# Kernel tuning notes

Measured on AMD Instinct MI355X. Metric: run time of the kernel, lower is better.

Reference implementation:

```python
import jax, jax.numpy as jnp
import numpy as np

B, S, D = 2, 2048, 2048
H = 16
DH = D // H  # 128, head dim for q, also the single kv head dim
ROPE_BASE = 10000.0


def _rope_cos_sin(seq_len, dim, dtype):
    inv_freq = 1.0 / (ROPE_BASE ** (jnp.arange(0, dim, 2, dtype=jnp.float32) / dim))
    t = jnp.arange(seq_len, dtype=jnp.float32)
    freqs = jnp.outer(t, inv_freq)            # [S, dim/2]
    emb = jnp.concatenate([freqs, freqs], -1)  # [S, dim]
    return jnp.cos(emb).astype(dtype), jnp.sin(emb).astype(dtype)


def _rotate_half(x):
    x1, x2 = x[..., : x.shape[-1] // 2], x[..., x.shape[-1] // 2 :]
    return jnp.concatenate([-x2, x1], axis=-1)


def setup_inputs() -> dict:
    key = jax.random.key(0)
    ks = jax.random.split(key, 7)
    s = 0.02
    return {
        "x": jax.random.normal(ks[0], (B, S, D), jnp.float32),
        "q_weight": jax.random.normal(ks[1], (H * DH, D), jnp.float32) * s,
        "q_bias": jax.random.normal(ks[2], (H * DH,), jnp.float32) * s,
        "kv_weight": jax.random.normal(ks[3], (2 * DH, D), jnp.float32) * s,
        "kv_bias": jax.random.normal(ks[4], (2 * DH,), jnp.float32) * s,
        "o_weight": jax.random.normal(ks[5], (D, H * DH), jnp.float32) * s,
        "o_bias": jax.random.normal(ks[6], (D,), jnp.float32) * s,
    }


def reference(x, q_weight, q_bias, kv_weight, kv_bias, o_weight, o_bias):
    b, s, d = x.shape
    # fused-style MQA projections (torch F.linear: y = x @ W.T + b)
    q = x @ q_weight.T + q_bias                      # [B,S,H*DH]
    kv = x @ kv_weight.T + kv_bias                   # [B,S,2*DH]
    q = q.reshape(b, s, H, DH)
    k, v = kv[..., :DH], kv[..., DH:]                # [B,S,DH] single kv head

    # rotary embedding (GPT-NeoX / rotate_half style) on q and k
    cos, sin = _rope_cos_sin(s, DH, x.dtype)         # [S,DH]
    q = q * cos[None, :, None, :] + _rotate_half(q) * sin[None, :, None, :]
    k = k * cos[None, :, :] + _rotate_half(k) * sin[None, :, :]

    # causal MQA attention (flash_attn_varlen with full masks == dense causal)
    scale = 1.0 / jnp.sqrt(jnp.asarray(DH, x.dtype))
    scores = jnp.einsum("bqhd,bkd->bhqk", q, k) * scale   # [B,H,S,S]
    causal = jnp.tril(jnp.ones((s, s), bool))
    scores = jnp.where(causal[None, None], scores, jnp.asarray(-1e9, x.dtype))
    probs = jax.nn.softmax(scores, axis=-1)
    attn = jnp.einsum("bhqk,bkd->bqhd", probs, v)         # [B,S,H,DH]

    out = attn.reshape(b, s, H * DH) @ o_weight.T + o_bias
    return out
```

## Files before the change

### kernel.cpp

```cpp
#include <hip/hip_runtime.h>
#include <math.h>

constexpr int Bb  = 2;
constexpr int Ss  = 2048;
constexpr int Dd  = 2048;
constexpr int Hh  = 16;
constexpr int DHd = 128;
constexpr int BS  = Bb * Ss;
constexpr int NQKV = 2304;

typedef __bf16 bf16x8 __attribute__((ext_vector_type(8)));
typedef float  f32x4  __attribute__((ext_vector_type(4)));

static __device__ __forceinline__ unsigned short f2bf(float f) {
  union { float f; unsigned int u; } a; a.f = f;
  unsigned int u = a.u;
  unsigned int r = (u + 0x7fffu + ((u >> 16) & 1u)) >> 16;
  return (unsigned short)r;
}
static __device__ __forceinline__ float bf2f(unsigned short u) {
  union { unsigned int u; float f; } a; a.u = ((unsigned int)u) << 16;
  return a.f;
}
static __device__ __forceinline__ int pk2bf(float lo, float hi) {
  return (int)((unsigned int)f2bf(lo) | ((unsigned int)f2bf(hi) << 16));
}
static __device__ __forceinline__ f32x4 mfma16(bf16x8 a, bf16x8 b, f32x4 c) {
  return __builtin_amdgcn_mfma_f32_16x16x32_bf16(a, b, c, 0, 0, 0);
}

__global__ __launch_bounds__(256) void cast_all(
    const float* __restrict__ qw, const float* __restrict__ kvw,
    const float* __restrict__ ow, const float* __restrict__ x,
    unsigned short* __restrict__ dst,
    float2* __restrict__ ctab)
{
  const int blk = blockIdx.x;
  if (blk >= 16896) {
    const int id = (blk - 16896) * 256 + threadIdx.x;
    const int s = id >> 6, i = id & 63;
    const float invf = exp2f(-(float)i * (13.287712379549449f / 64.0f));
    const float ang = (float)s * invf;
    ctab[id] = make_float2(cosf(ang), sinf(ang));
    return;
  }
  const int i = blk * 256 + threadIdx.x;
  const float* src; int off;
  if (i < 1048576)      { src = qw;  off = 0; }
  else if (i < 1179648) { src = kvw; off = 1048576; }
  else if (i < 2228224) { src = ow;  off = 1179648; }
  else                  { src = x;   off = 2228224; }
  const float4 v = ((const float4*)src)[i - off];
  ushort4 o;
  o.x = f2bf(v.x); o.y = f2bf(v.y); o.z = f2bf(v.z); o.w = f2bf(v.w);
  ((ushort4*)dst)[i] = o;
}

#define TM 128
#define TN 128
#define TK 32

#define GLOAD16(gp, lp)                                                        \
  __builtin_amdgcn_global_load_lds(                                            \
      (const __attribute__((address_space(1))) void*)(gp),                     \
      (__attribute__((address_space(3))) void*)(lp), 16, 0, 0)

template <bool BF16OUT>
__global__ __launch_bounds__(256) void gemm_bt_mfma(
    const unsigned short* __restrict__ A,
    const unsigned short* __restrict__ Bw,
    const float* __restrict__ bias1,
    const float* __restrict__ bias2,
    int nsplit,
    void* __restrict__ Cv,
    int M, int N, int K)
{
  __shared__ unsigned short As[TM * TK];
  __shared__ unsigned short Bs[TN * TK];

  const int tid  = threadIdx.x;
  const int w    = tid >> 6;
  const int lane = tid & 63;
  const int m0   = blockIdx.y * TM;
  const int n0   = blockIdx.x * TN;
  const int wm   = (w >> 1) * 64;
  const int wn   = (w & 1) * 64;

  f32x4 acc[4][4];
#pragma unroll
  for (int i = 0; i < 4; i++)
#pragma unroll
    for (int j = 0; j < 4; j++) acc[i][j] = (f32x4){0.f, 0.f, 0.f, 0.f};

  const int srow = lane >> 2;
  const int scol = (lane & 3) * 8;
  const unsigned short* aG0 = A  + (size_t)(m0 +      w * 16 + srow) * K + scol;
  const unsigned short* aG1 = A  + (size_t)(m0 + 64 + w * 16 + srow) * K + scol;
  const unsigned short* bG0 = Bw + (size_t)(n0 +      w * 16 + srow) * K + scol;
  const unsigned short* bG1 = Bw + (size_t)(n0 + 64 + w * 16 + srow) * K + scol;
  unsigned short* aL0 = &As[(     w * 16) * TK];
  unsigned short* aL1 = &As[(64 + w * 16) * TK];
  unsigned short* bL0 = &Bs[(     w * 16) * TK];
  unsigned short* bL1 = &Bs[(64 + w * 16) * TK];

  const int fr = lane & 15;
  const int fk = (lane >> 4) * 8;

  for (int k0 = 0; k0 < K; k0 += TK) {
    __syncthreads();
    GLOAD16(aG0 + k0, aL0);
    GLOAD16(aG1 + k0, aL1);
    GLOAD16(bG0 + k0, bL0);
    GLOAD16(bG1 + k0, bL1);
    __syncthreads();

    bf16x8 af[4], bfr[4];
#pragma unroll
    for (int i = 0; i < 4; i++)
      af[i] = *(const bf16x8*)&As[(wm + i * 16 + fr) * TK + fk];
#pragma unroll
    for (int j = 0; j < 4; j++)
      bfr[j] = *(const bf16x8*)&Bs[(wn + j * 16 + fr) * TK + fk];
#pragma unroll
    for (int i = 0; i < 4; i++)
#pragma unroll
      for (int j = 0; j < 4; j++)
        acc[i][j] = mfma16(af[i], bfr[j], acc[i][j]);
  }

  const int er = (lane >> 4) * 4;
  const int ec = lane & 15;
#pragma unroll
  for (int j = 0; j < 4; j++) {
    const int col = n0 + wn + j * 16 + ec;
    const float bv = (col < nsplit) ? bias1[col] : bias2[col - nsplit];
#pragma unroll
    for (int i = 0; i < 4; i++) {
      const int rbase = m0 + wm + i * 16 + er;
#pragma unroll
      for (int r = 0; r < 4; r++) {
        const float v = acc[i][j][r] + bv;
        if constexpr (BF16OUT)
          ((unsigned short*)Cv)[(size_t)(rbase + r) * N + col] = f2bf(v);
        else
          ((float*)Cv)[(size_t)(rbase + r) * N + col] = v;
      }
    }
  }
}

__global__ __launch_bounds__(256) void prep_kv(
    const unsigned short* __restrict__ QKV,
    const float2* __restrict__ ctab,
    unsigned short* __restrict__ Kb,
    unsigned short* __restrict__ Vt)
{
  __shared__ unsigned short Vtile[64 * 136];

  const int blk = blockIdx.x;
  const int b   = blk >> 5;
  const int s0  = (blk & 31) * 64;
  const int t   = threadIdx.x;

  {
    const int r = t >> 2, p = t & 3;
    const int row = blk * 64 + r;
    const int s = row & (Ss - 1);
    const unsigned short* src = QKV + (size_t)row * NQKV + 2048 + p * 16;
    const float2* ct = ctab + s * 64 + p * 16;
    union { uint4 v[2]; unsigned short a[16]; } lo, hi, ol, oh;
    lo.v[0] = *(const uint4*)src;        lo.v[1] = *(const uint4*)(src + 8);
    hi.v[0] = *(const uint4*)(src + 64); hi.v[1] = *(const uint4*)(src + 72);
#pragma unroll
    for (int e = 0; e < 16; e++) {
      const float2 cs = ct[e];
      const float l = bf2f(lo.a[e]), hh = bf2f(hi.a[e]);
      ol.a[e] = f2bf(l * cs.x - hh * cs.y);
      oh.a[e] = f2bf(hh * cs.x + l * cs.y);
    }
    unsigned short* dst = Kb + (size_t)row * 128 + p * 16;
    *(uint4*)dst        = ol.v[0]; *(uint4*)(dst + 8)  = ol.v[1];
    *(uint4*)(dst + 64) = oh.v[0]; *(uint4*)(dst + 72) = oh.v[1];
  }

#pragma unroll
  for (int c = 0; c < 4; c++) {
    const int id = c * 256 + t;
    const int vr = id >> 4, cc = id & 15;
    *(uint4*)&Vtile[vr * 136 + cc * 8] =
        *(const uint4*)(QKV + (size_t)(blk * 64 + vr) * NQKV + 2176 + cc * 8);
  }
  __syncthreads();

  {
    const int d = t >> 1, half = t & 1;
    union { uint4 v[4]; unsigned short a[32]; } val;
#pragma unroll
    for (int kk = 0; kk < 32; kk++)
      val.a[kk] = Vtile[(half * 32 + kk) * 136 + d];
    unsigned short* dst = Vt + ((size_t)(b * 128 + d)) * Ss + s0 + half * 32;
#pragma unroll
    for (int c = 0; c < 4; c++) *(uint4*)(dst + c * 8) = val.v[c];
  }
}

__global__ __launch_bounds__(256, 4) void flash_v9(
    const unsigned short* __restrict__ QKV,
    const unsigned short* __restrict__ Kb,
    const unsigned short* __restrict__ Vt,
    const float2* __restrict__ ctab,
    unsigned short* __restrict__ attn)
{
  __shared__ unsigned short Ks[4 * 64 * 32];
  __shared__ unsigned short Vs[2 * 128 * 32];

  const int g   = (int)blockIdx.x;
  const int k4  = g >> 8;
  const int qtp = g & 31;
  const int m   = (g >> 5) & 7;
  const int hb  = m + 8 * k4;
  const int h   = hb & 15;
  const int b   = hb >> 4;
  const int q2  = (k4 & 2) ? ((qtp + 16) & 31) : qtp;
  const int qt  = (k4 & 1) ? (31 - q2) : q2;

  const int q0 = qt * 64;
  const int tid = threadIdx.x;
  const int w = tid >> 6, lane = tid & 63;
  const int lg = lane >> 4, lm = lane & 15;
  const int qrow = q0 + w * 16 + lm;
  const int qrow_hi = q0 + w * 16 + 15;

  const int klg = lg ^ ((lm >> 1) & 3);

  bf16x8 qf[4];
  {
    const unsigned short* qp =
        QKV + (size_t)(b * Ss + qrow) * NQKV + h * DHd + lg * 8;
    const float2* ct = ctab + qrow * 64 + lg * 8;
    union U8 { bf16x8 v; unsigned short a[8]; };
    U8 lo0, lo1, hi0, hi1, ol0, ol1, oh0, oh1;
    lo0.v = *(const bf16x8*)(qp);
    lo1.v = *(const bf16x8*)(qp + 32);
    hi0.v = *(const bf16x8*)(qp + 64);
    hi1.v = *(const bf16x8*)(qp + 96);
#pragma unroll
    for (int j = 0; j < 8; j++) {
      {
        const float2 cs = ct[j];
        const float l = bf2f(lo0.a[j]), hh = bf2f(hi0.a[j]);
        ol0.a[j] = f2bf(l * cs.x - hh * cs.y);
        oh0.a[j] = f2bf(hh * cs.x + l * cs.y);
      }
      {
        const float2 cs = ct[32 + j];
        const float l = bf2f(lo1.a[j]), hh = bf2f(hi1.a[j]);
        ol1.a[j] = f2bf(l * cs.x - hh * cs.y);
        oh1.a[j] = f2bf(hh * cs.x + l * cs.y);
      }
    }
    qf[0] = ol0.v; qf[1] = ol1.v; qf[2] = oh0.v; qf[3] = oh1.v;
  }

  f32x4 ot[8];
#pragma unroll
  for (int dt = 0; dt < 8; dt++) ot[dt] = (f32x4){0.f, 0.f, 0.f, 0.f};
  float lsum = 0.f;

  const float sscale = 0.08838834764831845f * 1.4426950408889634f;

  const int sr  = lane >> 2;
  const int sc8 = ((lane & 3) ^ ((lane >> 3) & 3)) * 8;
  const unsigned short* kg =
      Kb + (size_t)b * Ss * 128 + (size_t)sr * 128 + w * 32 + sc8;
  const unsigned short* vg =
      Vt + (size_t)b * 128 * Ss + (size_t)(w * 32 + sr) * Ss + sc8;
  unsigned short* ksl  = &Ks[w * 2048];
  unsigned short* vsl0 = &Vs[(w * 32) * 32];
  unsigned short* vsl1 = &Vs[4096 + (w * 32) * 32];

  const int addr0 = (2 * (lg & 1)) * 16 + lm;
  const int addr1 = addr0 + 16;
  const bool sel_hi = (lg & 2) != 0;

  auto half32 = [&](int keybase, int tA, const unsigned short* VsP) {
    f32x4 s[2];
    s[0] = (f32x4){0.f, 0.f, 0.f, 0.f};
    s[1] = (f32x4){0.f, 0.f, 0.f, 0.f};
#pragma unroll
    for (int kf = 0; kf < 4; kf++) {
      const bf16x8 k0 = *(const bf16x8*)&Ks[kf * 2048 + ((tA)     * 16 + lm) * 32 + klg * 8];
      const bf16x8 k1 = *(const bf16x8*)&Ks[kf * 2048 + ((tA + 1) * 16 + lm) * 32 + klg * 8];
      s[0] = mfma16(k0, qf[kf], s[0]);
      s[1] = mfma16(k1, qf[kf], s[1]);
    }
    int pk[2][2];
#pragma unroll
    for (int t = 0; t < 2; t++) {
      float p[4];
#pragma unroll
      for (int r = 0; r < 4; r++) {
        const int key = keybase + t * 16 + 4 * lg + r;
        const float ev = exp2f(s[t][r] * sscale);
        p[r] = (key <= qrow) ? ev : 0.f;
        lsum += p[r];
      }
      pk[t][0] = pk2bf(p[0], p[1]);
      pk[t][1] = pk2bf(p[2], p[3]);
    }
    union { int d[4]; bf16x8 v; } pb;
#pragma unroll
    for (int d = 0; d < 4; d++) {
      const int src = (d < 2) ? addr0 : addr1;
      const int v0 = __shfl(pk[0][d & 1], src);
      const int v1 = __shfl(pk[1][d & 1], src);
      pb.d[d] = sel_hi ? v1 : v0;
    }
#pragma unroll
    for (int dt = 0; dt < 8; dt++) {
      const bf16x8 vfrag = *(const bf16x8*)&VsP[(dt * 16 + lm) * 32 + klg * 8];
      ot[dt] = mfma16(vfrag, pb.v, ot[dt]);
    }
  };

  for (int j0 = 0; j0 <= q0; j0 += 64) {
    __syncthreads();
#pragma unroll
    for (int i = 0; i < 4; i++)
      GLOAD16(kg + (size_t)(j0 + i * 16) * 128, ksl + i * 512);
#pragma unroll
    for (int i = 0; i < 2; i++) {
      GLOAD16(vg + (size_t)(i * 16) * Ss + j0,      vsl0 + i * 512);
      GLOAD16(vg + (size_t)(i * 16) * Ss + j0 + 32, vsl1 + i * 512);
    }
    __syncthreads();

    half32(j0, 0, &Vs[0]);
    if (j0 + 32 <= qrow_hi)
      half32(j0 + 32, 2, &Vs[4096]);
  }

  lsum += __shfl_xor(lsum, 16);
  lsum += __shfl_xor(lsum, 32);
  const float inv = 1.0f / lsum;

  unsigned short* dst = attn + (size_t)(b * Ss + qrow) * Dd + h * DHd + lg * 4;
#pragma unroll
  for (int dt = 0; dt < 8; dt++) {
    ushort4 o4;
    o4.x = f2bf(ot[dt][0] * inv);
    o4.y = f2bf(ot[dt][1] * inv);
    o4.z = f2bf(ot[dt][2] * inv);
    o4.w = f2bf(ot[dt][3] * inv);
    *(ushort4*)(dst + dt * 16) = o4;
  }
}

extern "C" void kernel_launch(void* const* d_in, const int* in_sizes, int n_in,
                              void* d_out, int out_size, void* d_ws, size_t ws_size,
                              hipStream_t stream) {
  const float* x   = (const float*)d_in[0];
  const float* qw  = (const float*)d_in[1];
  const float* qb  = (const float*)d_in[2];
  const float* kvw = (const float*)d_in[3];
  const float* kvb = (const float*)d_in[4];
  const float* ow  = (const float*)d_in[5];
  const float* ob  = (const float*)d_in[6];
  float* out = (float*)d_out;

  unsigned short* wsb    = (unsigned short*)d_ws;
  unsigned short* wqkv   = wsb;
  unsigned short* owb    = wsb + 4718592;
  unsigned short* xb     = wsb + 8912896;
  unsigned short* attn_b = xb;
  unsigned short* QKV    = wsb + 17301504;
  unsigned short* Kb     = wsb + 26738688;
  unsigned short* Vt     = wsb + 27262976;
  float2*         ctab   = (float2*)(wsb + 27787264);

  cast_all<<<17408, 256, 0, stream>>>(qw, kvw, ow, x, wqkv, ctab);

  gemm_bt_mfma<true><<<dim3(NQKV / TN, BS / TM), 256, 0, stream>>>(
      xb, wqkv, qb, kvb, 2048, QKV, BS, NQKV, Dd);

  prep_kv<<<BS / 64, 256, 0, stream>>>(QKV, ctab, Kb, Vt);

  flash_v9<<<1024, 256, 0, stream>>>(QKV, Kb, Vt, ctab, attn_b);

  gemm_bt_mfma<false><<<dim3(Dd / TN, BS / TM), 256, 0, stream>>>(
      attn_b, owb, ob, ob, Dd, out, BS, Dd, Dd);
}
```

Before: 317.7 us.

## Process paired causal query tiles per block sharing 128-key K/V loads

The flash attention kernel now gives each block two query tiles (p and 31-p) that share each K/V tile loaded into shared memory, and the key step grows from 64 to 128. Pairing tiles this way balances causal work across blocks and halves the K/V global-to-LDS traffic per query tile. The cost is twice the accumulator registers, doubled shared memory, fewer resident blocks (launch bounds 2) and half the grid size, so occupancy and latency hiding drop.

```diff
diff --git a/kernel.cpp b/kernel.cpp
--- a/kernel.cpp
+++ b/kernel.cpp
@@ -204,68 +204,77 @@
   }
 }
 
-__global__ __launch_bounds__(256, 4) void flash_v9(
+__global__ __launch_bounds__(256, 2) void flash_v10(
     const unsigned short* __restrict__ QKV,
     const unsigned short* __restrict__ Kb,
     const unsigned short* __restrict__ Vt,
     const float2* __restrict__ ctab,
     unsigned short* __restrict__ attn)
 {
-  __shared__ unsigned short Ks[4 * 64 * 32];
-  __shared__ unsigned short Vs[2 * 128 * 32];
-
-  const int g   = (int)blockIdx.x;
-  const int k4  = g >> 8;
-  const int qtp = g & 31;
-  const int m   = (g >> 5) & 7;
-  const int hb  = m + 8 * k4;
-  const int h   = hb & 15;
-  const int b   = hb >> 4;
-  const int q2  = (k4 & 2) ? ((qtp + 16) & 31) : qtp;
-  const int qt  = (k4 & 1) ? (31 - q2) : q2;
-
-  const int q0 = qt * 64;
+  __shared__ unsigned short Ks[4 * 128 * 32];
+  __shared__ unsigned short Vs[4 * 128 * 32];
+
+  const int g  = (int)blockIdx.x;
+  const int lo = g & 255, hi = g >> 8;
+  const int p  = hi ? (15 - (lo & 15)) : (lo & 15);
+  const int hb = (lo >> 4) + 16 * hi;
+  const int h  = hb & 15;
+  const int b  = hb >> 4;
+
+  const int qA0 = (31 - p) * 64;
+  const int qB0 = p * 64;
+
   const int tid = threadIdx.x;
   const int w = tid >> 6, lane = tid & 63;
   const int lg = lane >> 4, lm = lane & 15;
-  const int qrow = q0 + w * 16 + lm;
-  const int qrow_hi = q0 + w * 16 + 15;
+  const int qrowA = qA0 + w * 16 + lm;
+  const int qrowA_hi = qA0 + w * 16 + 15;
+  const int qrowB = qB0 + w * 16 + lm;
+  const int qrowB_hi = qB0 + w * 16 + 15;
 
   const int klg = lg ^ ((lm >> 1) & 3);
 
-  bf16x8 qf[4];
+  bf16x8 qfA[4], qfB[4];
   {
-    const unsigned short* qp =
-        QKV + (size_t)(b * Ss + qrow) * NQKV + h * DHd + lg * 8;
-    const float2* ct = ctab + qrow * 64 + lg * 8;
     union U8 { bf16x8 v; unsigned short a[8]; };
-    U8 lo0, lo1, hi0, hi1, ol0, ol1, oh0, oh1;
-    lo0.v = *(const bf16x8*)(qp);
-    lo1.v = *(const bf16x8*)(qp + 32);
-    hi0.v = *(const bf16x8*)(qp + 64);
-    hi1.v = *(const bf16x8*)(qp + 96);
-#pragma unroll
-    for (int j = 0; j < 8; j++) {
-      {
-        const float2 cs = ct[j];
-        const float l = bf2f(lo0.a[j]), hh = bf2f(hi0.a[j]);
-        ol0.a[j] = f2bf(l * cs.x - hh * cs.y);
-        oh0.a[j] = f2bf(hh * cs.x + l * cs.y);
+#pragma unroll
+    for (int tile = 0; tile < 2; tile++) {
+      const int qrow = tile ? qrowB : qrowA;
+      const unsigned short* qp =
+          QKV + (size_t)(b * Ss + qrow) * NQKV + h * DHd + lg * 8;
+      const float2* ct = ctab + qrow * 64 + lg * 8;
+      U8 lo0, lo1, hi0, hi1, ol0, ol1, oh0, oh1;
+      lo0.v = *(const bf16x8*)(qp);
+      lo1.v = *(const bf16x8*)(qp + 32);
+      hi0.v = *(const bf16x8*)(qp + 64);
+      hi1.v = *(const bf16x8*)(qp + 96);
+#pragma unroll
+      for (int j = 0; j < 8; j++) {
+        {
+          const float2 cs = ct[j];
+          const float l = bf2f(lo0.a[j]), hh = bf2f(hi0.a[j]);
+          ol0.a[j] = f2bf(l * cs.x - hh * cs.y);
+          oh0.a[j] = f2bf(hh * cs.x + l * cs.y);
+        }
+        {
+          const float2 cs = ct[32 + j];
+          const float l = bf2f(lo1.a[j]), hh = bf2f(hi1.a[j]);
+          ol1.a[j] = f2bf(l * cs.x - hh * cs.y);
+          oh1.a[j] = f2bf(hh * cs.x + l * cs.y);
+        }
       }
-      {
-        const float2 cs = ct[32 + j];
-        const float l = bf2f(lo1.a[j]), hh = bf2f(hi1.a[j]);
-        ol1.a[j] = f2bf(l * cs.x - hh * cs.y);
-        oh1.a[j] = f2bf(hh * cs.x + l * cs.y);
-      }
-    }
-    qf[0] = ol0.v; qf[1] = ol1.v; qf[2] = oh0.v; qf[3] = oh1.v;
-  }
-
-  f32x4 ot[8];
-#pragma unroll
-  for (int dt = 0; dt < 8; dt++) ot[dt] = (f32x4){0.f, 0.f, 0.f, 0.f};
-  float lsum = 0.f;
+      if (tile == 0) { qfA[0]=ol0.v; qfA[1]=ol1.v; qfA[2]=oh0.v; qfA[3]=oh1.v; }
+      else           { qfB[0]=ol0.v; qfB[1]=ol1.v; qfB[2]=oh0.v; qfB[3]=oh1.v; }
+    }
+  }
+
+  f32x4 otA[8], otB[8];
+#pragma unroll
+  for (int dt = 0; dt < 8; dt++) {
+    otA[dt] = (f32x4){0.f, 0.f, 0.f, 0.f};
+    otB[dt] = (f32x4){0.f, 0.f, 0.f, 0.f};
+  }
+  float lsumA = 0.f, lsumB = 0.f;
 
   const float sscale = 0.08838834764831845f * 1.4426950408889634f;
 
@@ -275,38 +284,38 @@
       Kb + (size_t)b * Ss * 128 + (size_t)sr * 128 + w * 32 + sc8;
   const unsigned short* vg =
       Vt + (size_t)b * 128 * Ss + (size_t)(w * 32 + sr) * Ss + sc8;
-  unsigned short* ksl  = &Ks[w * 2048];
-  unsigned short* vsl0 = &Vs[(w * 32) * 32];
-  unsigned short* vsl1 = &Vs[4096 + (w * 32) * 32];
+  unsigned short* ksl = &Ks[w * 4096];
 
   const int addr0 = (2 * (lg & 1)) * 16 + lm;
   const int addr1 = addr0 + 16;
   const bool sel_hi = (lg & 2) != 0;
 
-  auto half32 = [&](int keybase, int tA, const unsigned short* VsP) {
+  auto half32 = [&](int keybase, int tA, const unsigned short* VsP,
+                    const bf16x8 (&qf)[4], f32x4 (&ot)[8], float& lsum,
+                    int qrow) {
     f32x4 s[2];
     s[0] = (f32x4){0.f, 0.f, 0.f, 0.f};
     s[1] = (f32x4){0.f, 0.f, 0.f, 0.f};
 #pragma unroll
     for (int kf = 0; kf < 4; kf++) {
-      const bf16x8 k0 = *(const bf16x8*)&Ks[kf * 2048 + ((tA)     * 16 + lm) * 32 + klg * 8];
-      const bf16x8 k1 = *(const bf16x8*)&Ks[kf * 2048 + ((tA + 1) * 16 + lm) * 32 + klg * 8];
+      const bf16x8 k0 = *(const bf16x8*)&Ks[kf * 4096 + ((tA)     * 16 + lm) * 32 + klg * 8];
+      const bf16x8 k1 = *(const bf16x8*)&Ks[kf * 4096 + ((tA + 1) * 16 + lm) * 32 + klg * 8];
       s[0] = mfma16(k0, qf[kf], s[0]);
       s[1] = mfma16(k1, qf[kf], s[1]);
     }
     int pk[2][2];
 #pragma unroll
     for (int t = 0; t < 2; t++) {
-      float p[4];
+      float pv[4];
 #pragma unroll
       for (int r = 0; r < 4; r++) {
         const int key = keybase + t * 16 + 4 * lg + r;
         const float ev = exp2f(s[t][r] * sscale);
-        p[r] = (key <= qrow) ? ev : 0.f;
-        lsum += p[r];
+        pv[r] = (key <= qrow) ? ev : 0.f;
+        lsum += pv[r];
       }
-      pk[t][0] = pk2bf(p[0], p[1]);
-      pk[t][1] = pk2bf(p[2], p[3]);
+      pk[t][0] = pk2bf(pv[0], pv[1]);
+      pk[t][1] = pk2bf(pv[2], pv[3]);
     }
     union { int d[4]; bf16x8 v; } pb;
 #pragma unroll
@@ -323,36 +332,58 @@
     }
   };
 
-  for (int j0 = 0; j0 <= q0; j0 += 64) {
+  for (int j0 = 0; j0 <= qA0; j0 += 128) {
     __syncthreads();
 #pragma unroll
-    for (int i = 0; i < 4; i++)
+    for (int i = 0; i < 8; i++)
       GLOAD16(kg + (size_t)(j0 + i * 16) * 128, ksl + i * 512);
 #pragma unroll
-    for (int i = 0; i < 2; i++) {
-      GLOAD16(vg + (size_t)(i * 16) * Ss + j0,      vsl0 + i * 512);
-      GLOAD16(vg + (size_t)(i * 16) * Ss + j0 + 32, vsl1 + i * 512);
+    for (int ks2 = 0; ks2 < 4; ks2++) {
+      unsigned short* vsl = &Vs[ks2 * 4096 + (w * 32) * 32];
+      GLOAD16(vg + j0 + ks2 * 32,                  vsl);
+      GLOAD16(vg + (size_t)16 * Ss + j0 + ks2 * 32, vsl + 512);
     }
     __syncthreads();
 
-    half32(j0, 0, &Vs[0]);
-    if (j0 + 32 <= qrow_hi)
-      half32(j0 + 32, 2, &Vs[4096]);
-  }
-
-  lsum += __shfl_xor(lsum, 16);
-  lsum += __shfl_xor(lsum, 32);
-  const float inv = 1.0f / lsum;
-
-  unsigned short* dst = attn + (size_t)(b * Ss + qrow) * Dd + h * DHd + lg * 4;
-#pragma unroll
-  for (int dt = 0; dt < 8; dt++) {
-    ushort4 o4;
-    o4.x = f2bf(ot[dt][0] * inv);
-    o4.y = f2bf(ot[dt][1] * inv);
-    o4.z = f2bf(ot[dt][2] * inv);
-    o4.w = f2bf(ot[dt][3] * inv);
-    *(ushort4*)(dst + dt * 16) = o4;
+    half32(j0, 0, &Vs[0], qfA, otA, lsumA, qrowA);
+    if (j0 + 32 <= qrowA_hi)
+      half32(j0 + 32, 2, &Vs[4096], qfA, otA, lsumA, qrowA);
+    if (j0 + 64 <= qA0) {
+      half32(j0 + 64, 4, &Vs[8192], qfA, otA, lsumA, qrowA);
+      if (j0 + 96 <= qrowA_hi)
+        half32(j0 + 96, 6, &Vs[12288], qfA, otA, lsumA, qrowA);
+    }
+    if (j0 <= qB0) {
+      half32(j0, 0, &Vs[0], qfB, otB, lsumB, qrowB);
+      if (j0 + 32 <= qrowB_hi)
+        half32(j0 + 32, 2, &Vs[4096], qfB, otB, lsumB, qrowB);
+      if (j0 + 64 <= qB0) {
+        half32(j0 + 64, 4, &Vs[8192], qfB, otB, lsumB, qrowB);
+        if (j0 + 96 <= qrowB_hi)
+          half32(j0 + 96, 6, &Vs[12288], qfB, otB, lsumB, qrowB);
+      }
+    }
+  }
+
+#pragma unroll
+  for (int tile = 0; tile < 2; tile++) {
+    float lsum = tile ? lsumB : lsumA;
+    const int qrow = tile ? qrowB : qrowA;
+    lsum += __shfl_xor(lsum, 16);
+    lsum += __shfl_xor(lsum, 32);
+    const float inv = 1.0f / lsum;
+    unsigned short* dst =
+        attn + (size_t)(b * Ss + qrow) * Dd + h * DHd + lg * 4;
+#pragma unroll
+    for (int dt = 0; dt < 8; dt++) {
+      const f32x4 o = tile ? otB[dt] : otA[dt];
+      ushort4 o4;
+      o4.x = f2bf(o[0] * inv);
+      o4.y = f2bf(o[1] * inv);
+      o4.z = f2bf(o[2] * inv);
+      o4.w = f2bf(o[3] * inv);
+      *(ushort4*)(dst + dt * 16) = o4;
+    }
   }
 }
 
@@ -385,7 +416,7 @@
 
   prep_kv<<<BS / 64, 256, 0, stream>>>(QKV, ctab, Kb, Vt);
 
-  flash_v9<<<1024, 256, 0, stream>>>(QKV, Kb, Vt, ctab, attn_b);
+  flash_v10<<<512, 256, 0, stream>>>(QKV, Kb, Vt, ctab, attn_b);
 
   gemm_bt_mfma<false><<<dim3(Dd / TN, BS / TM), 256, 0, stream>>>(
       attn_b, owb, ob, ob, Dd, out, BS, Dd, Dd);
```

Measured after the change: 307.8 us. 3.1% less time.
